# Kernel optimization log

Hardware: AMD Instinct MI355X
Metric: run time of the kernel (lower is better)

Reference implementation:

```python
import jax, jax.numpy as jnp
import numpy as np

END_CLAUSE, PRED, ARG_FUNC, ARG_VAR = 0, 1, 2, 3
NUM_ACTION_TYPES = 8
NUM_LAYERS = 3


def _ln(x, g, b, eps=1e-5):
    m = jnp.mean(x, -1, keepdims=True)
    v = jnp.var(x, -1, keepdims=True)
    return (x - m) * jax.lax.rsqrt(v + eps) * g + b


def _ssm_block(x, Win, b_in, Wdt, b_dt, Alog, WB, b_B, WC, b_C, Dp, Wout, b_out, g, b):
    # x: [B,T,D]
    res = x
    xz = x @ Win.T + b_in
    x_ssm, z = jnp.split(xz, 2, axis=-1)
    z = jax.nn.silu(z)
    dt = jax.nn.softplus(x_ssm @ Wdt.T + b_dt)   # [B,T,D]
    Bm = x_ssm @ WB.T + b_B                       # [B,T,N]
    Cm = x_ssm @ WC.T + b_C                       # [B,T,N]
    A = -jnp.exp(Alog)                            # [D,N]

    def step(h, inp):
        x_t, dt_t, B_t, C_t = inp                 # [B,D],[B,D],[B,N],[B,N]
        dA = jnp.exp(A[None] * dt_t[:, :, None])  # [B,D,N]
        h = dA * h + (dt_t * x_t)[:, :, None] * B_t[:, None, :]
        return h, jnp.einsum('bdn,bn->bd', h, C_t)

    h0 = jnp.zeros((x.shape[0], Alog.shape[0], Alog.shape[1]), x.dtype)
    xs = tuple(jnp.swapaxes(a, 0, 1) for a in (x_ssm, dt, Bm, Cm))
    _, ys = jax.lax.scan(step, h0, xs)
    y = jnp.swapaxes(ys, 0, 1)                    # [B,T,D]
    y = (y + Dp * x_ssm) * z
    y = y @ Wout.T + b_out
    return _ln(y + res, g, b)


def _forward(symbol_embeds, memory, action_embed, W_arg, b_arg, var_embed, W_comb, b_comb,
             Win, b_in, Wdt, b_dt, Alog, WB, b_B, WC, b_C, Dp, Wout, b_out, ssm_g, ssm_b,
             Wm, b_m, Wg, b_g, cn_g, cn_b, Wa, b_a, Wq, b_q, Wk, b_k, Wv, b_v,
             target_actions, target_arguments, symbol_mask):
    B, T = target_actions.shape
    S = symbol_embeds.shape[1]
    D = symbol_embeds.shape[2]
    MV = var_embed.shape[0]
    # teacher-forcing shift with END_CLAUSE BOS
    dec_a = jnp.concatenate([jnp.full((B, 1), END_CLAUSE, target_actions.dtype), target_actions[:, :-1]], 1)
    dec_g = jnp.concatenate([jnp.zeros((B, 1), target_arguments.dtype), target_arguments[:, :-1]], 1)
    act_emb = action_embed[dec_a]                                          # [B,T,D]
    sym = symbol_embeds[jnp.arange(B)[:, None], jnp.clip(dec_g, 0, S - 1)]  # [B,T,D]
    ptr_emb = sym @ W_arg.T + b_arg
    var_emb_t = var_embed[jnp.clip(dec_g, 0, MV - 1)]
    ptr_mask = (dec_a == PRED) | (dec_a == ARG_FUNC)
    vmask = dec_a == ARG_VAR
    arg_emb = jnp.where(ptr_mask[..., None], ptr_emb,
                        jnp.where(vmask[..., None], var_emb_t, jnp.zeros((), symbol_embeds.dtype)))
    h = jnp.concatenate([act_emb, arg_emb], -1) @ W_comb.T + b_comb
    mem_summary = memory.mean(1)  # zero padding included, matching torch code
    for l in range(NUM_LAYERS):
        h = _ssm_block(h, Win[l], b_in[l], Wdt[l], b_dt[l], Alog[l], WB[l], b_B[l], WC[l], b_C[l],
                       Dp[l], Wout[l], b_out[l], ssm_g[l], ssm_b[l])
        ctx = jnp.broadcast_to((mem_summary @ Wm[l].T + b_m[l])[:, None, :], h.shape)
        gate = jax.nn.sigmoid(jnp.concatenate([h, ctx], -1) @ Wg[l].T + b_g[l])
        h = _ln(h + gate * ctx, cn_g[l], cn_b[l])
    action_logits = h @ Wa.T + b_a
    scores = jnp.einsum('btd,bsd->bts', h @ Wq.T + b_q, symbol_embeds @ Wk.T + b_k) / (float(D) ** 0.5)
    scores = jnp.where(symbol_mask[:, None, :], scores, -jnp.inf)
    var_logits = h @ Wv.T + b_v
    return action_logits, scores, var_logits


def setup_inputs() -> dict:
    B, T, S, M, D, N, L, NA, MV = 8, 1024, 128, 512, 512, 16, NUM_LAYERS, NUM_ACTION_TYPES, 20
    keys = iter(jax.random.split(jax.random.key(0), 48))

    def nrm(shape, scale=1.0):
        return jax.random.normal(next(keys), shape, jnp.float32) * scale

    s = 1.0 / np.sqrt(D)
    s2 = 1.0 / np.sqrt(2 * D)
    inp = dict(
        symbol_embeds=nrm((B, S, D)), memory=nrm((B, M, D)),
        action_embed=nrm((NA, D), 0.02), W_arg=nrm((D, D), s), b_arg=jnp.zeros((D,)),
        var_embed=nrm((MV, D), 0.02), W_comb=nrm((D, 2 * D), s2), b_comb=jnp.zeros((D,)),
        Win=nrm((L, 2 * D, D), s), b_in=jnp.zeros((L, 2 * D)),
        Wdt=nrm((L, D, D), s), b_dt=jnp.zeros((L, D)),
        Alog=nrm((L, D, N)),
        WB=nrm((L, N, D), s), b_B=jnp.zeros((L, N)),
        WC=nrm((L, N, D), s), b_C=jnp.zeros((L, N)),
        Dp=jnp.ones((L, D)),
        Wout=nrm((L, D, D), s), b_out=jnp.zeros((L, D)),
        ssm_g=jnp.ones((L, D)), ssm_b=jnp.zeros((L, D)),
        Wm=nrm((L, D, D), s), b_m=jnp.zeros((L, D)),
        Wg=nrm((L, D, 2 * D), s2), b_g=jnp.zeros((L, D)),
        cn_g=jnp.ones((L, D)), cn_b=jnp.zeros((L, D)),
        Wa=nrm((NA, D), s), b_a=jnp.zeros((NA,)),
        Wq=nrm((D, D), s), b_q=jnp.zeros((D,)),
        Wk=nrm((D, D), s), b_k=jnp.zeros((D,)),
        Wv=nrm((MV, D), s), b_v=jnp.zeros((MV,)),
        target_actions=jax.random.randint(next(keys), (B, T), 0, NA),
        target_arguments=jax.random.randint(next(keys), (B, T), 0, S),
    )
    counts = jax.random.randint(next(keys), (B,), S // 2, S + 1)
    inp['symbol_mask'] = jnp.arange(S)[None, :] < counts[:, None]
    return inp


def reference(symbol_embeds, memory, action_embed, W_arg, b_arg, var_embed, W_comb, b_comb,
              Win, b_in, Wdt, b_dt, Alog, WB, b_B, WC, b_C, Dp, Wout, b_out, ssm_g, ssm_b,
              Wm, b_m, Wg, b_g, cn_g, cn_b, Wa, b_a, Wq, b_q, Wk, b_k, Wv, b_v,
              target_actions, target_arguments, symbol_mask):
    return _forward(symbol_embeds, memory, action_embed, W_arg, b_arg, var_embed, W_comb, b_comb,
                    Win, b_in, Wdt, b_dt, Alog, WB, b_B, WC, b_C, Dp, Wout, b_out, ssm_g, ssm_b,
                    Wm, b_m, Wg, b_g, cn_g, cn_b, Wa, b_a, Wq, b_q, Wk, b_k, Wv, b_v,
                    target_actions, target_arguments, symbol_mask)
```

## Files before the change

### kernel.cpp

```cpp
#include <hip/hip_runtime.h>
#include <math.h>

#define R_  8192
#define T_  1024
#define B_  8
#define S_  128
#define D_  512
#define N_  16
#define MV_ 20
#define NA_ 8
#define MM_ 512

#define TC  4
#define LCH 256
#define TS  32
#define DB  8
#define TP  36

typedef __attribute__((ext_vector_type(8))) short short8;
typedef __attribute__((ext_vector_type(4))) float f32x4;

static __device__ __forceinline__ float sigmoidf_(float x) {
  return 1.f / (1.f + __expf(-x));
}

static __device__ __forceinline__ void split2(float x0, float x1,
                                              unsigned& hp, unsigned& lp) {
  unsigned u0 = __float_as_uint(x0), u1 = __float_as_uint(x1);
  unsigned r0 = u0 + 0x7fffu + ((u0 >> 16) & 1u);
  unsigned r1 = u1 + 0x7fffu + ((u1 >> 16) & 1u);
  hp = __builtin_amdgcn_perm(r1, r0, 0x07060302u);
  float l0 = x0 - __uint_as_float(r0 & 0xffff0000u);
  float l1 = x1 - __uint_as_float(r1 & 0xffff0000u);
  lp = __builtin_amdgcn_perm(__float_as_uint(l1), __float_as_uint(l0),
                             0x07060302u);
}

#define KP 40

__global__ void __launch_bounds__(256) gemm_bx3(
    const float* __restrict__ A, int lda,
    const unsigned short* __restrict__ Wh, const unsigned short* __restrict__ Wl,
    const float* __restrict__ bias,
    const float* __restrict__ bbias,
    float* __restrict__ C, int ldc,
    int K, int act,
    float* __restrict__ aux1, float* __restrict__ aux2)
{
  __shared__ unsigned short Ah[128 * KP], Al[128 * KP];
  __shared__ unsigned short Bh[64 * KP],  Bl[64 * KP];
  const int tid = threadIdx.x;
  const int m0 = blockIdx.y << 7;
  const int n0 = blockIdx.x << 6;
  const int lane = tid & 63;
  const int wm = ((tid >> 6) & 1) << 6;
  const int wn = (tid >> 7) << 5;
  const int lr = lane & 15, quad = lane >> 4;

  const int arow = tid >> 1, akoff = (tid & 1) << 4;
  const float* ap = A + (size_t)(m0 + arow) * lda + akoff;
  const int brow = tid >> 2, bkoff = (tid & 3) << 3;
  const unsigned short* wph = Wh + (size_t)(n0 + brow) * K + bkoff;
  const unsigned short* wpl = Wl + (size_t)(n0 + brow) * K + bkoff;

  f32x4 acc[4][2];
#pragma unroll
  for (int mt = 0; mt < 4; ++mt)
#pragma unroll
    for (int nt = 0; nt < 2; ++nt)
      acc[mt][nt] = (f32x4){0.f, 0.f, 0.f, 0.f};

  for (int k0 = 0; k0 < K; k0 += 32) {
    float4 av[4];
#pragma unroll
    for (int i = 0; i < 4; ++i) av[i] = *(const float4*)(ap + k0 + (i << 2));
    uint4 bh = *(const uint4*)(wph + k0);
    uint4 bl = *(const uint4*)(wpl + k0);
    __syncthreads();
    {
      float af[16] = {av[0].x, av[0].y, av[0].z, av[0].w,
                      av[1].x, av[1].y, av[1].z, av[1].w,
                      av[2].x, av[2].y, av[2].z, av[2].w,
                      av[3].x, av[3].y, av[3].z, av[3].w};
#pragma unroll
      for (int g = 0; g < 2; ++g) {
        unsigned h4[4], l4[4];
#pragma unroll
        for (int p = 0; p < 4; ++p)
          split2(af[g * 8 + 2 * p], af[g * 8 + 2 * p + 1], h4[p], l4[p]);
        *(uint4*)&Ah[arow * KP + akoff + (g << 3)] = make_uint4(h4[0], h4[1], h4[2], h4[3]);
        *(uint4*)&Al[arow * KP + akoff + (g << 3)] = make_uint4(l4[0], l4[1], l4[2], l4[3]);
      }
    }
    *(uint4*)&Bh[brow * KP + bkoff] = bh;
    *(uint4*)&Bl[brow * KP + bkoff] = bl;
    __syncthreads();

    short8 fah[4], fal[4], fbh[2], fbl[2];
#pragma unroll
    for (int mt = 0; mt < 4; ++mt) {
      int r = (wm + mt * 16 + lr) * KP + quad * 8;
      fah[mt] = *(const short8*)&Ah[r];
      fal[mt] = *(const short8*)&Al[r];
    }
#pragma unroll
    for (int nt = 0; nt < 2; ++nt) {
      int r = (wn + nt * 16 + lr) * KP + quad * 8;
      fbh[nt] = *(const short8*)&Bh[r];
      fbl[nt] = *(const short8*)&Bl[r];
    }
#pragma unroll
    for (int mt = 0; mt < 4; ++mt)
#pragma unroll
      for (int nt = 0; nt < 2; ++nt) {
        acc[mt][nt] = __builtin_amdgcn_mfma_f32_16x16x32_bf16(
            fah[mt], fbl[nt], acc[mt][nt], 0, 0, 0);
        acc[mt][nt] = __builtin_amdgcn_mfma_f32_16x16x32_bf16(
            fal[mt], fbh[nt], acc[mt][nt], 0, 0, 0);
        acc[mt][nt] = __builtin_amdgcn_mfma_f32_16x16x32_bf16(
            fah[mt], fbh[nt], acc[mt][nt], 0, 0, 0);
      }
  }

  const int bb = m0 >> 10;
#pragma unroll
  for (int mt = 0; mt < 4; ++mt)
#pragma unroll
    for (int nt = 0; nt < 2; ++nt) {
      int ncol = n0 + wn + nt * 16 + lr;
      float bv = bias ? bias[ncol] : 0.f;
      if (bbias) bv += bbias[(size_t)bb * ldc + ncol];
#pragma unroll
      for (int reg = 0; reg < 4; ++reg) {
        int m = m0 + wm + mt * 16 + quad * 4 + reg;
        float v = acc[mt][nt][reg] + bv;
        if (act == 0) {
          C[(size_t)m * ldc + ncol] = v;
        } else if (act == 1) {
          C[(size_t)m * ldc + ncol] = (v > 20.f) ? v : log1pf(__expf(v));
        } else if (act == 2) {
          C[(size_t)m * ldc + ncol] = sigmoidf_(v);
        } else if (act == 3) {
          if (ncol < 512)      C[(size_t)m * 512 + ncol] = (v > 20.f) ? v : log1pf(__expf(v));
          else if (ncol < 528) aux1[(size_t)m * 16 + (ncol - 512)] = v;
          else if (ncol < 544) aux2[(size_t)m * 16 + (ncol - 528)] = v;
        } else {
          if (ncol < 512)      C[(size_t)m * 512 + ncol] = v;
          else if (ncol < 520) aux1[(size_t)m * 8 + (ncol - 512)] = v;
          else if (ncol < 540) aux2[(size_t)m * 20 + (ncol - 520)] = v;
        }
      }
    }
}

static __device__ __forceinline__ void wcvt_body(
    int gid, const float* __restrict__ W, int ldw,
    unsigned short* __restrict__ hi, unsigned short* __restrict__ lo)
{
  int base = gid << 3;
  int r = base >> 9, c = base & 511;
  const float* p = W + (size_t)r * ldw + c;
  float4 a0 = *(const float4*)p, a1 = *(const float4*)(p + 4);
  float af[8] = {a0.x, a0.y, a0.z, a0.w, a1.x, a1.y, a1.z, a1.w};
  unsigned h4[4], l4[4];
#pragma unroll
  for (int p2 = 0; p2 < 4; ++p2) split2(af[2 * p2], af[2 * p2 + 1], h4[p2], l4[p2]);
  *(uint4*)&hi[(size_t)r * 512 + c] = make_uint4(h4[0], h4[1], h4[2], h4[3]);
  *(uint4*)&lo[(size_t)r * 512 + c] = make_uint4(l4[0], l4[1], l4[2], l4[3]);
}

static __device__ __forceinline__ void pack_body(
    int gid, unsigned short* __restrict__ hi, unsigned short* __restrict__ lo,
    float* __restrict__ bd,
    const float* __restrict__ w0, const float* __restrict__ b0,
    const float* __restrict__ w1, const float* __restrict__ b1,
    const float* __restrict__ w2, const float* __restrict__ b2,
    int n1, int n2)
{
  int base = gid << 3;
  int r = base >> 9, c = base & 511;
  const float* src = nullptr;
  if (r < 512)                 src = w0 + (size_t)r * 512 + c;
// ... 38 lines not shown
                           const float* __restrict__ Wg_l,
                           unsigned short* WsqH, unsigned short* WsqL,
                           unsigned short* WgH, unsigned short* WgL)
{
  int blk = blockIdx.x;
  if (blk < 128)
    wcvt_body(blk * 256 + threadIdx.x, Wout_l, 512, WsqH, WsqL);
  else
    wcvt_body((blk - 128) * 256 + threadIdx.x, Wg_l, 1024, WgH, WgL);
}

__global__ void cvt_heads(const float* __restrict__ Wq, const float* __restrict__ b_q,
                          const float* __restrict__ Wa, const float* __restrict__ b_a,
                          const float* __restrict__ Wv, const float* __restrict__ b_v,
                          const float* __restrict__ Wk,
                          unsigned short* WpkH, unsigned short* WpkL, float* bpk,
                          unsigned short* WsqH, unsigned short* WsqL)
{
  int blk = blockIdx.x;
  if (blk < 144)
    pack_body(blk * 256 + threadIdx.x, WpkH, WpkL, bpk,
              Wq, b_q, Wa, b_a, Wv, b_v, NA_, MV_);
  else
    wcvt_body((blk - 144) * 256 + threadIdx.x, Wk, 512, WsqH, WsqL);
}

__global__ void wcvt(const float* __restrict__ W, int ldw,
                     unsigned short* __restrict__ hi, unsigned short* __restrict__ lo)
{
  wcvt_body(blockIdx.x * 256 + threadIdx.x, W, ldw, hi, lo);
}

#define BM 64
#define BN 64
#define BK 16

__global__ void __launch_bounds__(256) scores_kernel(
    const float* __restrict__ q, const float* __restrict__ kmat,
    const int* __restrict__ mask, float* __restrict__ out)
{
  __shared__ __align__(16) float As[BK][BM + 4];
  __shared__ __align__(16) float Ws[BK][BN + 4];
  const int b = blockIdx.z;
  const float* A = q + (size_t)b * T_ * D_;
  const float* W = kmat + (size_t)b * S_ * D_;
  const int tid = threadIdx.x;
  const int m0 = blockIdx.y * BM;
  const int n0 = blockIdx.x * BN;
  const int tx = tid & 15, ty = tid >> 4;
  const int lr = tid >> 2;
  const int lk = (tid & 3) << 2;
  float acc[4][4] = {{0.f}};
  const float* aptr = A + (size_t)(m0 + lr) * D_ + lk;
  const float* wptr = W + (size_t)(n0 + lr) * D_ + lk;

  for (int k0 = 0; k0 < D_; k0 += BK) {
    float4 av = *(const float4*)(aptr + k0);
    float4 wv = *(const float4*)(wptr + k0);
    __syncthreads();
    As[lk + 0][lr] = av.x; As[lk + 1][lr] = av.y;
    As[lk + 2][lr] = av.z; As[lk + 3][lr] = av.w;
    Ws[lk + 0][lr] = wv.x; Ws[lk + 1][lr] = wv.y;
    Ws[lk + 2][lr] = wv.z; Ws[lk + 3][lr] = wv.w;
    __syncthreads();
#pragma unroll
    for (int kk = 0; kk < BK; ++kk) {
      float4 a4 = *(const float4*)&As[kk][ty << 2];
      float4 b4 = *(const float4*)&Ws[kk][tx << 2];
      float a_[4] = {a4.x, a4.y, a4.z, a4.w};
      float b_[4] = {b4.x, b4.y, b4.z, b4.w};
#pragma unroll
      for (int i = 0; i < 4; ++i)
#pragma unroll
        for (int j = 0; j < 4; ++j)
          acc[i][j] = fmaf(a_[i], b_[j], acc[i][j]);
    }
  }

  const float scale = 0.044194173824159216f;
#pragma unroll
  for (int i = 0; i < 4; ++i) {
    int t = m0 + (ty << 2) + i;
#pragma unroll
    for (int j = 0; j < 4; ++j) {
      int s = n0 + (tx << 2) + j;
      float v = acc[i][j] * scale;
      if (mask[b * S_ + s] == 0) v = -1e30f;
      out[((size_t)(b * T_ + t)) * S_ + s] = v;
    }
  }
}

__global__ void gemm_small(const float* __restrict__ A, int lda,
                           const float* __restrict__ W, int ldw,
                           const float* __restrict__ bias,
                           float* __restrict__ C, int ldc,
                           int MN, int Ncols, int K)
{
  int gid = blockIdx.x * 256 + threadIdx.x;
// ... 35 lines not shown
  float acc = b_g[l * 512 + dd];
  for (int k = 0; k < 128; ++k) {
    float4 av = a[k], wv = w[k];
    acc = fmaf(av.x, wv.x, fmaf(av.y, wv.y, fmaf(av.z, wv.z, fmaf(av.w, wv.w, acc))));
  }
  gctx[gid] = acc;
}

__global__ void __launch_bounds__(256) transpose512(
    const float* __restrict__ A, float* __restrict__ At)
{
  __shared__ float tl[32][33];
  int i0 = blockIdx.y * 32, j0 = blockIdx.x * 32;
  int li = threadIdx.x & 31, lj = threadIdx.x >> 5;
#pragma unroll
  for (int k = 0; k < 4; ++k)
    tl[lj * 4 + k][li] = A[(size_t)(i0 + lj * 4 + k) * 512 + j0 + li];
  __syncthreads();
#pragma unroll
  for (int k = 0; k < 4; ++k)
    At[(size_t)(j0 + lj * 4 + k) * 512 + i0 + li] = tl[li][lj * 4 + k];
}

__global__ void memsum_kernel(const float* __restrict__ mem, float* __restrict__ out)
{
  int b = blockIdx.x >> 1;
  int d = ((blockIdx.x & 1) << 8) + threadIdx.x;
  const float* p = mem + (size_t)b * MM_ * D_ + d;
  float s = 0.f;
  for (int m = 0; m < MM_; ++m) s += p[(size_t)m * D_];
  out[b * D_ + d] = s * (1.f / MM_);
}

__global__ void combine_kernel(float* __restrict__ h, const float* __restrict__ Psym,
                               const float* __restrict__ Pact,
                               const float* __restrict__ Pvar, const float* __restrict__ b2,
                               const float* __restrict__ bcomb,
                               const int* __restrict__ ta, const int* __restrict__ tg)
{
  int i = blockIdx.x * 256 + threadIdx.x;
  int r = i >> 9, j = i & 511;
  int t = r & (T_ - 1);
  int a = t ? ta[r - 1] : 0;
  float val = Pact[a * D_ + j] + bcomb[j];
  if (a == 1 || a == 2) {
    int g = t ? tg[r - 1] : 0;
    g = g < 0 ? 0 : (g > S_ - 1 ? S_ - 1 : g);
    val += Psym[((size_t)(r >> 10) * S_ + g) * D_ + j] + b2[j];
  } else if (a == 3) {
    int g = t ? tg[r - 1] : 0;
    g = g < 0 ? 0 : (g > MV_ - 1 ? MV_ - 1 : g);
    val += Pvar[g * D_ + j];
  }
  h[i] = val;
}

__global__ void __launch_bounds__(128) scan_pass1(
    const float* __restrict__ xz, const float* __restrict__ dts,
    const float* __restrict__ Bmv, const float* __restrict__ Alog,
    float* __restrict__ aprod, float* __restrict__ hend)
{
  __shared__ __align__(16) float sdtT[DB][TP];
  __shared__ __align__(16) float sxT[DB][TP];
  __shared__ __align__(16) float sB[TS][16];
  const int tid = threadIdx.x;
  const int n = tid & 15, dl = tid >> 4;
  const int c = blockIdx.x, db = blockIdx.y, b = blockIdx.z;
  const int d = (db << 3) + dl;
  const int t0 = c * LCH;
  const int lrow = tid >> 2, lc2 = (tid & 3) << 1, bc4 = (tid & 3) << 2;

  float An = -__expf(Alog[d * N_ + n]);
  float hst = 0.f, dsum = 0.f;

  for (int tt = 0; tt < LCH; tt += TS) {
    __syncthreads();
    {
      size_t gr = (size_t)b * T_ + t0 + tt + lrow;
      float2 dt2 = *(const float2*)&dts[(gr << 9) + (db << 3) + lc2];
      float2 x2  = *(const float2*)&xz[(gr << 10) + (db << 3) + lc2];
      sdtT[lc2][lrow] = dt2.x; sdtT[lc2 + 1][lrow] = dt2.y;
      sxT[lc2][lrow]  = x2.x;  sxT[lc2 + 1][lrow]  = x2.y;
      *(float4*)&sB[lrow][bc4] = *(const float4*)&Bmv[gr * N_ + bc4];
    }
    __syncthreads();
    float dtr[TS], xr[TS];
#pragma unroll
    for (int qv = 0; qv < TS / 4; ++qv) {
      *(float4*)&dtr[qv << 2] = *(const float4*)&sdtT[dl][qv << 2];
      *(float4*)&xr[qv << 2]  = *(const float4*)&sxT[dl][qv << 2];
    }
#pragma unroll
    for (int s = 0; s < TS; ++s) {
      float Bv = sB[s][n];
      float dA = __expf(An * dtr[s]);
      hst = fmaf(dA, hst, dtr[s] * xr[s] * Bv);
      dsum += dtr[s];
    }
  }
  size_t idx = (size_t)c * (B_ * D_ * N_) + ((size_t)b * D_ + d) * N_ + n;
  aprod[idx] = __expf(An * dsum);
  hend[idx]  = hst;
}

__global__ void scan_pass2(const float* __restrict__ aprod, float* __restrict__ hs)
{
  int g = blockIdx.x * 256 + threadIdx.x;
  float prev = 0.f;
  for (int c = 0; c < TC; ++c) {
    size_t idx = (size_t)c * (B_ * D_ * N_) + g;
    float a = aprod[idx], he = hs[idx];
    hs[idx] = prev;
    prev = fmaf(a, prev, he);
  }
}

#define HPAD 20

__global__ void __launch_bounds__(128) scan_pass3(
    const float* __restrict__ xz, float* __restrict__ dy,
    const float* __restrict__ Bmv, const float* __restrict__ Cmv,
    const float* __restrict__ Alog, const float* __restrict__ hstart,
    const float* __restrict__ Dp)
{
  __shared__ __align__(16) float sdtT[DB][TP];
  __shared__ __align__(16) float sxT[DB][TP];
  __shared__ __align__(16) float szT[DB][TP];
  __shared__ __align__(16) float sB[TS][16];
  __shared__ __align__(16) float sC[TS][16];
  __shared__ __align__(16) float sterm[128][HPAD];
  const int tid = threadIdx.x;
  const int n = tid & 15, dl = tid >> 4;
  const int c = blockIdx.x, db = blockIdx.y, b = blockIdx.z;
  const int d = (db << 3) + dl;
  const int t0 = c * LCH;
  const int lrow = tid >> 2, lc2 = (tid & 3) << 1, bc4 = (tid & 3) << 2;
  const int rsi = tid >> 3, rdl = tid & 7;

  float An = -__expf(Alog[d * N_ + n]);
  float Dpr = Dp[(db << 3) + rdl];
  size_t sidx = (size_t)c * (B_ * D_ * N_) + ((size_t)b * D_ + d) * N_ + n;
  float hst = hstart[sidx];

  for (int tt = 0; tt < LCH; tt += TS) {
    __syncthreads();
    {
      size_t gr = (size_t)b * T_ + t0 + tt + lrow;
      float2 dt2 = *(const float2*)&dy[(gr << 9) + (db << 3) + lc2];
      float2 x2  = *(const float2*)&xz[(gr << 10) + (db << 3) + lc2];
      float2 z2  = *(const float2*)&xz[(gr << 10) + D_ + (db << 3) + lc2];
      sdtT[lc2][lrow] = dt2.x; sdtT[lc2 + 1][lrow] = dt2.y;
      sxT[lc2][lrow]  = x2.x;  sxT[lc2 + 1][lrow]  = x2.y;
      szT[lc2][lrow]  = z2.x;  szT[lc2 + 1][lrow]  = z2.y;
      *(float4*)&sB[lrow][bc4] = *(const float4*)&Bmv[gr * N_ + bc4];
      *(float4*)&sC[lrow][bc4] = *(const float4*)&Cmv[gr * N_ + bc4];
    }
    __syncthreads();
    float dtr[TS], xr[TS];
#pragma unroll
    for (int qv = 0; qv < TS / 4; ++qv) {
      *(float4*)&dtr[qv << 2] = *(const float4*)&sdtT[dl][qv << 2];
      *(float4*)&xr[qv << 2]  = *(const float4*)&sxT[dl][qv << 2];
    }
#pragma unroll
    for (int half = 0; half < 2; ++half) {
      const int hs = half << 4;
#pragma unroll
      for (int si = 0; si < 16; ++si) {
        int s = hs + si;
        float Bv = sB[s][n], Cv = sC[s][n];
        float dA = __expf(An * dtr[s]);
        hst = fmaf(dA, hst, dtr[s] * xr[s] * Bv);
        sterm[(si << 3) + dl][n] = hst * Cv;
      }
      __syncthreads();
      {
        float4 t0v = *(const float4*)&sterm[tid][0];
        float4 t1v = *(const float4*)&sterm[tid][4];
        float4 t2v = *(const float4*)&sterm[tid][8];
        float4 t3v = *(const float4*)&sterm[tid][12];
        float s16 = ((t0v.x + t0v.y) + (t0v.z + t0v.w))
                  + ((t1v.x + t1v.y) + (t1v.z + t1v.w))
                  + ((t2v.x + t2v.y) + (t2v.z + t2v.w))
                  + ((t3v.x + t3v.y) + (t3v.z + t3v.w));
        float zv = szT[rdl][hs + rsi];
        float xv = sxT[rdl][hs + rsi];
        float yv = (s16 + Dpr * xv) * (zv * sigmoidf_(zv));
        __syncthreads();
        sdtT[rdl][hs + rsi] = yv;
      }
      __syncthreads();
    }
    {
      size_t gr = (size_t)b * T_ + t0 + tt + lrow;
      float2 y2;
      y2.x = sdtT[lc2][lrow];
      y2.y = sdtT[lc2 + 1][lrow];
      *(float2*)&dy[(gr << 9) + (db << 3) + lc2] = y2;
    }
  }
}

__global__ void __launch_bounds__(256) ln_kernel(
    float* __restrict__ h, const float* __restrict__ add,
    const float* __restrict__ ctx,
    const float* __restrict__ gw, const float* __restrict__ bw, int mode)
{
  int r = (blockIdx.x << 2) + (threadIdx.x >> 6);
  int lane = threadIdx.x & 63;
  int b = r >> 10;
  size_t base = (size_t)r * D_;
  float v[8];
#pragma unroll
  for (int k = 0; k < 8; ++k) {
    int j = lane + (k << 6);
    float x = h[base + j];
    float a = add[base + j];
    v[k] = mode ? fmaf(a, ctx[b * D_ + j], x) : (x + a);
  }
  float s = 0.f;
#pragma unroll
  for (int k = 0; k < 8; ++k) s += v[k];
#pragma unroll
  for (int o = 1; o < 64; o <<= 1) s += __shfl_xor(s, o, 64);
  float mean = s * (1.f / D_);
  float vs = 0.f;
#pragma unroll
  for (int k = 0; k < 8; ++k) { float dv = v[k] - mean; vs = fmaf(dv, dv, vs); }
#pragma unroll
  for (int o = 1; o < 64; o <<= 1) vs += __shfl_xor(vs, o, 64);
  float inv = 1.0f / sqrtf(vs * (1.f / D_) + 1e-5f);
#pragma unroll
  for (int k = 0; k < 8; ++k) {
    int j = lane + (k << 6);
    h[base + j] = (v[k] - mean) * inv * gw[j] + bw[j];
  }
}

extern "C" void kernel_launch(void* const* d_in, const int* in_sizes, int n_in,
                              void* d_out, int out_size, void* d_ws, size_t ws_size,
                              hipStream_t stream)
{
  const float* symbol_embeds = (const float*)d_in[0];
  const float* memory_       = (const float*)d_in[1];
  const float* action_embed  = (const float*)d_in[2];
  const float* W_arg  = (const float*)d_in[3];
  const float* b_arg  = (const float*)d_in[4];
  const float* var_embed = (const float*)d_in[5];
  const float* W_comb = (const float*)d_in[6];
  const float* b_comb = (const float*)d_in[7];
  const float* Win  = (const float*)d_in[8];
  const float* b_in = (const float*)d_in[9];
  const float* Wdt  = (const float*)d_in[10];
  const float* b_dt = (const float*)d_in[11];
  const float* Alog = (const float*)d_in[12];
  const float* WB   = (const float*)d_in[13];
  const float* b_B  = (const float*)d_in[14];
  const float* WC   = (const float*)d_in[15];
  const float* b_C  = (const float*)d_in[16];
  const float* Dp   = (const float*)d_in[17];
  const float* Wout = (const float*)d_in[18];
  const float* b_out= (const float*)d_in[19];
  const float* ssm_g= (const float*)d_in[20];
  const float* ssm_b= (const float*)d_in[21];
  const float* Wm   = (const float*)d_in[22];
  const float* b_m  = (const float*)d_in[23];
  const float* Wg   = (const float*)d_in[24];
  const float* b_g  = (const float*)d_in[25];
  const float* cn_g = (const float*)d_in[26];
  const float* cn_b = (const float*)d_in[27];
  const float* Wa   = (const float*)d_in[28];
  const float* b_a  = (const float*)d_in[29];
  const float* Wq   = (const float*)d_in[30];
  const float* b_q  = (const float*)d_in[31];
  const float* Wk   = (const float*)d_in[32];
  const float* b_k  = (const float*)d_in[33];
  const float* Wv   = (const float*)d_in[34];
  const float* b_v  = (const float*)d_in[35];
  const int* ta     = (const int*)d_in[36];
  const int* tg     = (const int*)d_in[37];
  const int* smask  = (const int*)d_in[38];
  (void)in_sizes; (void)n_in; (void)out_size; (void)ws_size;

  float* ws = (float*)d_ws;
  float* xz = ws;
  float* dy = xz + (size_t)R_ * 1024;
  float* h  = dy + (size_t)R_ * 512;
  float* Psym = xz;

  float* out     = (float*)d_out;
  float* out_act = out;
  float* out_sc  = out + (size_t)R_ * NA_;
  float* out_var = out + (size_t)R_ * (NA_ + S_);

  float* Bmv  = out;
  float* Cmv  = Bmv  + 131072;
  float* aprd = Cmv  + 131072;
  float* hend = aprd + 262144;
  float* Wpk  = hend + 262144;
  float* bpk  = Wpk  + 294912;
  float* msum = bpk  + 576;
  float* ctxv = msum + 4096;
  float* gctx = ctxv + 12288;

  unsigned short* WpkH = (unsigned short*)Wpk;
  unsigned short* WpkL = WpkH + 294912;
  unsigned short* WinH = (unsigned short*)aprd;
  unsigned short* WinL = WinH + 524288;
  unsigned short* WsqH = (unsigned short*)aprd;
  unsigned short* WsqL = WsqH + 262144;
  unsigned short* WgH  = (unsigned short*)hend;
  unsigned short* WgL  = WgH + 262144;
  unsigned short* PrepH = (unsigned short*)Bmv;
  unsigned short* PrepL = PrepH + 262144;

  float* Pact = aprd;
  float* Pvar = Pact + 4096;
  float* b2   = Pvar + 10240;
  float* M2   = hend;
  float* WargT= Wpk;

  dim3 blk(256), blk128(128);

  memsum_kernel<<<16, blk, 0, stream>>>(memory_, msum);
  gemm_small<<<16, blk, 0, stream>>>(action_embed, 512, W_comb, 1024, nullptr,
                                     Pact, 512, 8 * 512, 512, 512);
  gemm_small<<<40, blk, 0, stream>>>(var_embed, 512, W_comb + 512, 1024, nullptr,
                                     Pvar, 512, 20 * 512, 512, 512);
  gemm_small<<<2, blk, 0, stream>>>(b_arg, 512, W_comb + 512, 1024, nullptr,
                                    b2, 512, 512, 512, 512);
  ctx_kernel<<<48, blk, 0, stream>>>(msum, Wm, b_m, ctxv);
  gctx_kernel<<<48, blk, 0, stream>>>(ctxv, Wg, b_g, gctx);
  transpose512<<<dim3(16, 16), blk, 0, stream>>>(W_arg, WargT);
  wcvt<<<128, blk, 0, stream>>>(WargT, 512, PrepH, PrepL);
  gemm_bx3<<<dim3(8, 4), blk, 0, stream>>>(W_comb + 512, 1024, PrepH, PrepL,
                                           nullptr, nullptr, M2, 512, 512, 0,
                                           nullptr, nullptr);
  wcvt<<<128, blk, 0, stream>>>(M2, 512, PrepH, PrepL);
  gemm_bx3<<<dim3(8, 8), blk, 0, stream>>>(symbol_embeds, 512, PrepH, PrepL,
                                           nullptr, nullptr, Psym, 512, 512, 0,
                                           nullptr, nullptr);
  combine_kernel<<<R_ * 512 / 256, blk, 0, stream>>>(h, Psym, Pact, Pvar, b2,
                                                     b_comb, ta, tg);

  for (int l = 0; l < 3; ++l) {
    const float* Win_l  = Win  + (size_t)l * 1024 * 512;
    const float* b_in_l = b_in + l * 1024;
    const float* Wdt_l  = Wdt  + (size_t)l * 512 * 512;
    const float* b_dt_l = b_dt + l * 512;
    const float* Alog_l = Alog + (size_t)l * 512 * 16;
    const float* WB_l   = WB   + (size_t)l * 16 * 512;
    const float* b_B_l  = b_B  + l * 16;
    const float* WC_l   = WC   + (size_t)l * 16 * 512;
    const float* b_C_l  = b_C  + l * 16;
    const float* Dp_l   = Dp   + l * 512;
    const float* Wout_l = Wout + (size_t)l * 512 * 512;
    const float* b_out_l= b_out+ l * 512;
    const float* ssm_g_l= ssm_g+ l * 512;
    const float* ssm_b_l= ssm_b+ l * 512;
    const float* Wg_l   = Wg   + (size_t)l * 512 * 1024;
    const float* cn_g_l = cn_g + l * 512;
    const float* cn_b_l = cn_b + l * 512;

    cvt_layerA<<<400, blk, 0, stream>>>(Win_l, Wdt_l, b_dt_l, WB_l, b_B_l,
                                        WC_l, b_C_l, WinH, WinL, WpkH, WpkL, bpk);
    gemm_bx3<<<dim3(16, 64), blk, 0, stream>>>(h, 512, WinH, WinL,
                                               b_in_l, nullptr, xz, 1024, 512, 0,
                                               nullptr, nullptr);
    gemm_bx3<<<dim3(9, 64), blk, 0, stream>>>(xz, 1024, WpkH, WpkL,
                                              bpk, nullptr, dy, 512, 512, 3,
                                              Bmv, Cmv);
    scan_pass1<<<dim3(TC, D_ / DB, B_), blk128, 0, stream>>>(xz, dy, Bmv, Alog_l,
                                                             aprd, hend);
    scan_pass2<<<B_ * D_ * N_ / 256, blk, 0, stream>>>(aprd, hend);
    scan_pass3<<<dim3(TC, D_ / DB, B_), blk128, 0, stream>>>(xz, dy, Bmv, Cmv,
                                                             Alog_l, hend, Dp_l);
    cvt_layerB<<<256, blk, 0, stream>>>(Wout_l, Wg_l, WsqH, WsqL, WgH, WgL);
    gemm_bx3<<<dim3(8, 64), blk, 0, stream>>>(dy, 512, WsqH, WsqL,
                                              b_out_l, nullptr, xz, 512, 512, 0,
                                              nullptr, nullptr);
    ln_kernel<<<2048, blk, 0, stream>>>(h, xz, nullptr, ssm_g_l, ssm_b_l, 0);
    gemm_bx3<<<dim3(8, 64), blk, 0, stream>>>(h, 512, WgH, WgL,
                                              nullptr, gctx + l * 4096, dy, 512, 512, 2,
                                              nullptr, nullptr);
    ln_kernel<<<2048, blk, 0, stream>>>(h, dy, ctxv + l * 4096, cn_g_l, cn_b_l, 1);
  }

  cvt_heads<<<272, blk, 0, stream>>>(Wq, b_q, Wa, b_a, Wv, b_v, Wk,
                                     WpkH, WpkL, bpk, WsqH, WsqL);
  gemm_bx3<<<dim3(9, 64), blk, 0, stream>>>(h, 512, WpkH, WpkL,
                                            bpk, nullptr, xz, 512, 512, 4,
                                            out_act, out_var);
  gemm_bx3<<<dim3(8, 8), blk, 0, stream>>>(symbol_embeds, 512, WsqH, WsqL,
                                           b_k, nullptr, dy, 512, 512, 0,
                                           nullptr, nullptr);
  scores_kernel<<<dim3(2, 16, 8), blk, 0, stream>>>(xz, dy, smask, out_sc);
}
```

Baseline: 1.171 ms.

## Store activations pre-split into bf16 hi/lo and widen GEMM tiles to 128

```diff
diff --git a/kernel.cpp b/kernel.cpp
--- a/kernel.cpp
+++ b/kernel.cpp
@@ -16,6 +16,7 @@
 #define TS  32
 #define DB  8
 #define TP  36
+#define KP  40
 
 typedef __attribute__((ext_vector_type(8))) short short8;
 typedef __attribute__((ext_vector_type(4))) float f32x4;
@@ -23,7 +24,13 @@
 static __device__ __forceinline__ float sigmoidf_(float x) {
   return 1.f / (1.f + __expf(-x));
 }
-
+static __device__ __forceinline__ void split1(float v, unsigned short& hi,
+                                              unsigned short& lo) {
+  unsigned u = __float_as_uint(v);
+  unsigned r = u + 0x7fffu + ((u >> 16) & 1u);
+  hi = (unsigned short)(r >> 16);
+  lo = (unsigned short)(__float_as_uint(v - __uint_as_float(r & 0xffff0000u)) >> 16);
+}
 static __device__ __forceinline__ void split2(float x0, float x1,
                                               unsigned& hp, unsigned& lp) {
   unsigned u0 = __float_as_uint(x0), u1 = __float_as_uint(x1);
@@ -35,68 +42,83 @@
   lp = __builtin_amdgcn_perm(__float_as_uint(l1), __float_as_uint(l0),
                              0x07060302u);
 }
-
-#define KP 40
-
-__global__ void __launch_bounds__(256) gemm_bx3(
-    const float* __restrict__ A, int lda,
+static __device__ __forceinline__ void recon2(unsigned hp, unsigned lp,
+                                              float& x0, float& x1) {
+  x0 = __uint_as_float(hp << 16) + __uint_as_float(lp << 16);
+  x1 = __uint_as_float(hp & 0xffff0000u) + __uint_as_float(lp & 0xffff0000u);
+}
+
+template<int BN>
+__global__ void __launch_bounds__(256) gemm_bb(
+    const unsigned short* __restrict__ Ahi, const unsigned short* __restrict__ Alo,
     const unsigned short* __restrict__ Wh, const unsigned short* __restrict__ Wl,
     const float* __restrict__ bias,
     const float* __restrict__ bbias,
     float* __restrict__ C, int ldc,
     int K, int act,
-    float* __restrict__ aux1, float* __restrict__ aux2)
+    float* __restrict__ aux1, float* __restrict__ aux2,
+    unsigned short* __restrict__ sp_hi, unsigned short* __restrict__ sp_lo)
 {
   __shared__ unsigned short Ah[128 * KP], Al[128 * KP];
-  __shared__ unsigned short Bh[64 * KP],  Bl[64 * KP];
+  __shared__ unsigned short Bh[BN * KP],  Bl[BN * KP];
   const int tid = threadIdx.x;
   const int m0 = blockIdx.y << 7;
-  const int n0 = blockIdx.x << 6;
+  const int n0 = blockIdx.x * BN;
   const int lane = tid & 63;
-  const int wm = ((tid >> 6) & 1) << 6;
-  const int wn = (tid >> 7) << 5;
+  const int widx = tid >> 6;
+  const int wm = (widx & 1) << 6;
+  const int wn = (widx >> 1) * (BN >> 1);
   const int lr = lane & 15, quad = lane >> 4;
+  const int NT = BN >> 5;
 
   const int arow = tid >> 1, akoff = (tid & 1) << 4;
-  const float* ap = A + (size_t)(m0 + arow) * lda + akoff;
-  const int brow = tid >> 2, bkoff = (tid & 3) << 3;
-  const unsigned short* wph = Wh + (size_t)(n0 + brow) * K + bkoff;
-  const unsigned short* wpl = Wl + (size_t)(n0 + brow) * K + bkoff;
-
-  f32x4 acc[4][2];
+  const unsigned short* aph = Ahi + (size_t)(m0 + arow) * K + akoff;
+  const unsigned short* apl = Alo + (size_t)(m0 + arow) * K + akoff;
+
+  f32x4 acc[4][4];
 #pragma unroll
   for (int mt = 0; mt < 4; ++mt)
 #pragma unroll
-    for (int nt = 0; nt < 2; ++nt)
+    for (int nt = 0; nt < NT; ++nt)
       acc[mt][nt] = (f32x4){0.f, 0.f, 0.f, 0.f};
 
   for (int k0 = 0; k0 < K; k0 += 32) {
-    float4 av[4];
-#pragma unroll
-    for (int i = 0; i < 4; ++i) av[i] = *(const float4*)(ap + k0 + (i << 2));
-    uint4 bh = *(const uint4*)(wph + k0);
-    uint4 bl = *(const uint4*)(wpl + k0);
+    uint4 ah0 = *(const uint4*)(aph + k0);
+    uint4 ah1 = *(const uint4*)(aph + k0 + 8);
+    uint4 al0 = *(const uint4*)(apl + k0);
+    uint4 al1 = *(const uint4*)(apl + k0 + 8);
+    uint4 bh0, bh1, bl0, bl1;
+    int brow, bkoff;
+    if (BN == 128) {
+      brow = tid >> 1; bkoff = (tid & 1) << 4;
+      const unsigned short* wph = Wh + (size_t)(n0 + brow) * K + bkoff;
+      const unsigned short* wpl = Wl + (size_t)(n0 + brow) * K + bkoff;
+      bh0 = *(const uint4*)(wph + k0); bh1 = *(const uint4*)(wph + k0 + 8);
+      bl0 = *(const uint4*)(wpl + k0); bl1 = *(const uint4*)(wpl + k0 + 8);
+    } else {
+      brow = tid >> 2; bkoff = (tid & 3) << 3;
+      const unsigned short* wph = Wh + (size_t)(n0 + brow) * K + bkoff;
+      const unsigned short* wpl = Wl + (size_t)(n0 + brow) * K + bkoff;
+      bh0 = *(const uint4*)(wph + k0);
+      bl0 = *(const uint4*)(wpl + k0);
+    }
     __syncthreads();
-    {
-      float af[16] = {av[0].x, av[0].y, av[0].z, av[0].w,
-                      av[1].x, av[1].y, av[1].z, av[1].w,
-                      av[2].x, av[2].y, av[2].z, av[2].w,
-                      av[3].x, av[3].y, av[3].z, av[3].w};
-#pragma unroll
-      for (int g = 0; g < 2; ++g) {
-        unsigned h4[4], l4[4];
-#pragma unroll
-        for (int p = 0; p < 4; ++p)
-          split2(af[g * 8 + 2 * p], af[g * 8 + 2 * p + 1], h4[p], l4[p]);
-        *(uint4*)&Ah[arow * KP + akoff + (g << 3)] = make_uint4(h4[0], h4[1], h4[2], h4[3]);
-        *(uint4*)&Al[arow * KP + akoff + (g << 3)] = make_uint4(l4[0], l4[1], l4[2], l4[3]);
-      }
-    }
-    *(uint4*)&Bh[brow * KP + bkoff] = bh;
-    *(uint4*)&Bl[brow * KP + bkoff] = bl;
+    *(uint4*)&Ah[arow * KP + akoff] = ah0;
+    *(uint4*)&Ah[arow * KP + akoff + 8] = ah1;
+    *(uint4*)&Al[arow * KP + akoff] = al0;
+    *(uint4*)&Al[arow * KP + akoff + 8] = al1;
+    if (BN == 128) {
+      *(uint4*)&Bh[brow * KP + bkoff] = bh0;
+      *(uint4*)&Bh[brow * KP + bkoff + 8] = bh1;
+      *(uint4*)&Bl[brow * KP + bkoff] = bl0;
+      *(uint4*)&Bl[brow * KP + bkoff + 8] = bl1;
+    } else {
+      *(uint4*)&Bh[brow * KP + bkoff] = bh0;
+      *(uint4*)&Bl[brow * KP + bkoff] = bl0;
+    }
     __syncthreads();
 
-    short8 fah[4], fal[4], fbh[2], fbl[2];
+    short8 fah[4], fal[4], fbh[4], fbl[4];
 #pragma unroll
     for (int mt = 0; mt < 4; ++mt) {
       int r = (wm + mt * 16 + lr) * KP + quad * 8;
@@ -104,7 +126,7 @@
       fal[mt] = *(const short8*)&Al[r];
     }
 #pragma unroll
-    for (int nt = 0; nt < 2; ++nt) {
+    for (int nt = 0; nt < NT; ++nt) {
       int r = (wn + nt * 16 + lr) * KP + quad * 8;
       fbh[nt] = *(const short8*)&Bh[r];
       fbl[nt] = *(const short8*)&Bl[r];
@@ -112,7 +134,7 @@
 #pragma unroll
     for (int mt = 0; mt < 4; ++mt)
 #pragma unroll
-      for (int nt = 0; nt < 2; ++nt) {
+      for (int nt = 0; nt < NT; ++nt) {
         acc[mt][nt] = __builtin_amdgcn_mfma_f32_16x16x32_bf16(
             fah[mt], fbl[nt], acc[mt][nt], 0, 0, 0);
         acc[mt][nt] = __builtin_amdgcn_mfma_f32_16x16x32_bf16(
@@ -126,7 +148,7 @@
 #pragma unroll
   for (int mt = 0; mt < 4; ++mt)
 #pragma unroll
-    for (int nt = 0; nt < 2; ++nt) {
+    for (int nt = 0; nt < NT; ++nt) {
       int ncol = n0 + wn + nt * 16 + lr;
       float bv = bias ? bias[ncol] : 0.f;
       if (bbias) bv += bbias[(size_t)bb * ldc + ncol];
@@ -136,18 +158,29 @@
         float v = acc[mt][nt][reg] + bv;
         if (act == 0) {
           C[(size_t)m * ldc + ncol] = v;
-        } else if (act == 1) {
-          C[(size_t)m * ldc + ncol] = (v > 20.f) ? v : log1pf(__expf(v));
         } else if (act == 2) {
           C[(size_t)m * ldc + ncol] = sigmoidf_(v);
         } else if (act == 3) {
-          if (ncol < 512)      C[(size_t)m * 512 + ncol] = (v > 20.f) ? v : log1pf(__expf(v));
+          if (ncol < 512) {
+            float sv = (v > 20.f) ? v : log1pf(__expf(v));
+            unsigned short hh, ll; split1(sv, hh, ll);
+            sp_hi[(size_t)m * 512 + ncol] = hh;
+            sp_lo[(size_t)m * 512 + ncol] = ll;
+          }
           else if (ncol < 528) aux1[(size_t)m * 16 + (ncol - 512)] = v;
           else if (ncol < 544) aux2[(size_t)m * 16 + (ncol - 528)] = v;
-        } else {
-          if (ncol < 512)      C[(size_t)m * 512 + ncol] = v;
+        } else if (act == 4) {
+          if (ncol < 512)      C[(size_t)m * ldc + ncol] = v;
           else if (ncol < 520) aux1[(size_t)m * 8 + (ncol - 512)] = v;
           else if (ncol < 540) aux2[(size_t)m * 20 + (ncol - 520)] = v;
+        } else {
+          if (ncol < 512) {
+            unsigned short hh, ll; split1(v, hh, ll);
+            sp_hi[(size_t)m * 512 + ncol] = hh;
+            sp_lo[(size_t)m * 512 + ncol] = ll;
+          } else {
+            aux2[(size_t)m * 512 + (ncol - 512)] = v;
+          }
         }
       }
     }
@@ -252,21 +285,21 @@
 }
 
 #define BM 64
-#define BN 64
-#define BK 16
+#define SBN 64
+#define SBK 16
 
 __global__ void __launch_bounds__(256) scores_kernel(
     const float* __restrict__ q, const float* __restrict__ kmat,
     const int* __restrict__ mask, float* __restrict__ out)
 {
-  __shared__ __align__(16) float As[BK][BM + 4];
-  __shared__ __align__(16) float Ws[BK][BN + 4];
+  __shared__ __align__(16) float As[SBK][BM + 4];
+  __shared__ __align__(16) float Ws[SBK][SBN + 4];
   const int b = blockIdx.z;
   const float* A = q + (size_t)b * T_ * D_;
   const float* W = kmat + (size_t)b * S_ * D_;
   const int tid = threadIdx.x;
   const int m0 = blockIdx.y * BM;
-  const int n0 = blockIdx.x * BN;
+  const int n0 = blockIdx.x * SBN;
   const int tx = tid & 15, ty = tid >> 4;
   const int lr = tid >> 2;
   const int lk = (tid & 3) << 2;
@@ -274,7 +307,7 @@
   const float* aptr = A + (size_t)(m0 + lr) * D_ + lk;
   const float* wptr = W + (size_t)(n0 + lr) * D_ + lk;
 
-  for (int k0 = 0; k0 < D_; k0 += BK) {
+  for (int k0 = 0; k0 < D_; k0 += SBK) {
     float4 av = *(const float4*)(aptr + k0);
     float4 wv = *(const float4*)(wptr + k0);
     __syncthreads();
@@ -284,7 +317,7 @@
     Ws[lk + 2][lr] = wv.z; Ws[lk + 3][lr] = wv.w;
     __syncthreads();
 #pragma unroll
-    for (int kk = 0; kk < BK; ++kk) {
+    for (int kk = 0; kk < SBK; ++kk) {
       float4 a4 = *(const float4*)&As[kk][ty << 2];
       float4 b4 = *(const float4*)&Ws[kk][tx << 2];
       float a_[4] = {a4.x, a4.y, a4.z, a4.w};
@@ -386,7 +419,10 @@
   out[b * D_ + d] = s * (1.f / MM_);
 }
 
-__global__ void combine_kernel(float* __restrict__ h, const float* __restrict__ Psym,
+__global__ void combine_kernel(float* __restrict__ h,
+                               unsigned short* __restrict__ sp_hi,
+                               unsigned short* __restrict__ sp_lo,
+                               const float* __restrict__ Psym,
                                const float* __restrict__ Pact,
                                const float* __restrict__ Pvar, const float* __restrict__ b2,
                                const float* __restrict__ bcomb,
@@ -407,10 +443,13 @@
     val += Pvar[g * D_ + j];
   }
   h[i] = val;
+  unsigned short hh, ll; split1(val, hh, ll);
+  sp_hi[i] = hh; sp_lo[i] = ll;
 }
 
 __global__ void __launch_bounds__(128) scan_pass1(
-    const float* __restrict__ xz, const float* __restrict__ dts,
+    const unsigned short* __restrict__ xhi, const unsigned short* __restrict__ xlo,
+    const unsigned short* __restrict__ dhi, const unsigned short* __restrict__ dlo,
     const float* __restrict__ Bmv, const float* __restrict__ Alog,
     float* __restrict__ aprod, float* __restrict__ hend)
 {
@@ -431,10 +470,16 @@
     __syncthreads();
     {
       size_t gr = (size_t)b * T_ + t0 + tt + lrow;
-      float2 dt2 = *(const float2*)&dts[(gr << 9) + (db << 3) + lc2];
-      float2 x2  = *(const float2*)&xz[(gr << 10) + (db << 3) + lc2];
-      sdtT[lc2][lrow] = dt2.x; sdtT[lc2 + 1][lrow] = dt2.y;
-      sxT[lc2][lrow]  = x2.x;  sxT[lc2 + 1][lrow]  = x2.y;
+      size_t ei = (gr << 9) + (db << 3) + lc2;
+      unsigned dh2 = *(const unsigned*)&dhi[ei];
+      unsigned dl2 = *(const unsigned*)&dlo[ei];
+      unsigned xh2 = *(const unsigned*)&xhi[ei];
+      unsigned xl2 = *(const unsigned*)&xlo[ei];
+      float d0, d1, x0, x1;
+      recon2(dh2, dl2, d0, d1);
+      recon2(xh2, xl2, x0, x1);
+      sdtT[lc2][lrow] = d0; sdtT[lc2 + 1][lrow] = d1;
+      sxT[lc2][lrow]  = x0; sxT[lc2 + 1][lrow]  = x1;
       *(float4*)&sB[lrow][bc4] = *(const float4*)&Bmv[gr * N_ + bc4];
     }
     __syncthreads();
@@ -472,7 +517,9 @@
 #define HPAD 20
 
 __global__ void __launch_bounds__(128) scan_pass3(
-    const float* __restrict__ xz, float* __restrict__ dy,
+    const unsigned short* __restrict__ xhi, const unsigned short* __restrict__ xlo,
+    unsigned short* __restrict__ dyhi, unsigned short* __restrict__ dylo,
+    const float* __restrict__ zreg,
     const float* __restrict__ Bmv, const float* __restrict__ Cmv,
     const float* __restrict__ Alog, const float* __restrict__ hstart,
     const float* __restrict__ Dp)
@@ -500,12 +547,18 @@
     __syncthreads();
     {
       size_t gr = (size_t)b * T_ + t0 + tt + lrow;
-      float2 dt2 = *(const float2*)&dy[(gr << 9) + (db << 3) + lc2];
-      float2 x2  = *(const float2*)&xz[(gr << 10) + (db << 3) + lc2];
-      float2 z2  = *(const float2*)&xz[(gr << 10) + D_ + (db << 3) + lc2];
-      sdtT[lc2][lrow] = dt2.x; sdtT[lc2 + 1][lrow] = dt2.y;
-      sxT[lc2][lrow]  = x2.x;  sxT[lc2 + 1][lrow]  = x2.y;
-      szT[lc2][lrow]  = z2.x;  szT[lc2 + 1][lrow]  = z2.y;
+      size_t ei = (gr << 9) + (db << 3) + lc2;
+      unsigned dh2 = *(const unsigned*)&dyhi[ei];
+      unsigned dl2 = *(const unsigned*)&dylo[ei];
+      unsigned xh2 = *(const unsigned*)&xhi[ei];
+      unsigned xl2 = *(const unsigned*)&xlo[ei];
+      float d0, d1, x0, x1;
+      recon2(dh2, dl2, d0, d1);
+      recon2(xh2, xl2, x0, x1);
+      float2 z2 = *(const float2*)&zreg[ei];
+      sdtT[lc2][lrow] = d0; sdtT[lc2 + 1][lrow] = d1;
+      sxT[lc2][lrow]  = x0; sxT[lc2 + 1][lrow]  = x1;
+      szT[lc2][lrow]  = z2.x; szT[lc2 + 1][lrow] = z2.y;
       *(float4*)&sB[lrow][bc4] = *(const float4*)&Bmv[gr * N_ + bc4];
       *(float4*)&sC[lrow][bc4] = *(const float4*)&Cmv[gr * N_ + bc4];
     }
@@ -547,16 +600,20 @@
     }
     {
       size_t gr = (size_t)b * T_ + t0 + tt + lrow;
-      float2 y2;
-      y2.x = sdtT[lc2][lrow];
-      y2.y = sdtT[lc2 + 1][lrow];
-      *(float2*)&dy[(gr << 9) + (db << 3) + lc2] = y2;
+      size_t ei = (gr << 9) + (db << 3) + lc2;
+      float y0 = sdtT[lc2][lrow], y1 = sdtT[lc2 + 1][lrow];
+      unsigned hp, lp;
+      split2(y0, y1, hp, lp);
+      *(unsigned*)&dyhi[ei] = hp;
+      *(unsigned*)&dylo[ei] = lp;
     }
   }
 }
 
 __global__ void __launch_bounds__(256) ln_kernel(
-    float* __restrict__ h, const float* __restrict__ add,
+    float* __restrict__ h,
+    unsigned short* __restrict__ sp_hi, unsigned short* __restrict__ sp_lo,
+    const float* __restrict__ add,
     const float* __restrict__ ctx,
     const float* __restrict__ gw, const float* __restrict__ bw, int mode)
 {
@@ -587,7 +644,10 @@
 #pragma unroll
   for (int k = 0; k < 8; ++k) {
     int j = lane + (k << 6);
-    h[base + j] = (v[k] - mean) * inv * gw[j] + bw[j];
+    float ov = (v[k] - mean) * inv * gw[j] + bw[j];
+    h[base + j] = ov;
+    unsigned short hh, ll; split1(ov, hh, ll);
+    sp_hi[base + j] = hh; sp_lo[base + j] = ll;
   }
 }
 
@@ -636,11 +696,16 @@
   const int* smask  = (const int*)d_in[38];
   (void)in_sizes; (void)n_in; (void)out_size; (void)ws_size;
 
+  const size_t RD = (size_t)R_ * 512;
+
   float* ws = (float*)d_ws;
-  float* xz = ws;
-  float* dy = xz + (size_t)R_ * 1024;
-  float* h  = dy + (size_t)R_ * 512;
-  float* Psym = xz;
+  unsigned short* xhi = (unsigned short*)ws;
+  unsigned short* xlo = xhi + RD;
+  float* regA = ws;
+  float* zreg = ws + RD;
+  unsigned short* csp_hi = (unsigned short*)(ws + 2 * RD);
+  unsigned short* csp_lo = csp_hi + RD;
+  float* h = ws + 3 * RD;
 
   float* out     = (float*)d_out;
   float* out_act = out;
@@ -660,7 +725,7 @@
   unsigned short* WpkH = (unsigned short*)Wpk;
   unsigned short* WpkL = WpkH + 294912;
   unsigned short* WinH = (unsigned short*)aprd;
-  unsigned short* WinL = WinH + 524288;
+  unsigned short* WinL = (unsigned short*)hend;
   unsigned short* WsqH = (unsigned short*)aprd;
   unsigned short* WsqL = WsqH + 262144;
   unsigned short* WgH  = (unsigned short*)hend;
@@ -687,15 +752,15 @@
   gctx_kernel<<<48, blk, 0, stream>>>(ctxv, Wg, b_g, gctx);
   transpose512<<<dim3(16, 16), blk, 0, stream>>>(W_arg, WargT);
   wcvt<<<128, blk, 0, stream>>>(WargT, 512, PrepH, PrepL);
-  gemm_bx3<<<dim3(8, 4), blk, 0, stream>>>(W_comb + 512, 1024, PrepH, PrepL,
-                                           nullptr, nullptr, M2, 512, 512, 0,
-                                           nullptr, nullptr);
+  wcvt<<<128, blk, 0, stream>>>(W_comb + 512, 1024, csp_hi, csp_lo);
+  gemm_bb<128><<<dim3(4, 4), blk, 0, stream>>>(csp_hi, csp_lo, PrepH, PrepL,
+      nullptr, nullptr, M2, 512, 512, 0, nullptr, nullptr, nullptr, nullptr);
   wcvt<<<128, blk, 0, stream>>>(M2, 512, PrepH, PrepL);
-  gemm_bx3<<<dim3(8, 8), blk, 0, stream>>>(symbol_embeds, 512, PrepH, PrepL,
-                                           nullptr, nullptr, Psym, 512, 512, 0,
-                                           nullptr, nullptr);
-  combine_kernel<<<R_ * 512 / 256, blk, 0, stream>>>(h, Psym, Pact, Pvar, b2,
-                                                     b_comb, ta, tg);
+  wcvt<<<256, blk, 0, stream>>>(symbol_embeds, 512, csp_hi, csp_lo);
+  gemm_bb<128><<<dim3(4, 8), blk, 0, stream>>>(csp_hi, csp_lo, PrepH, PrepL,
+      nullptr, nullptr, regA, 512, 512, 0, nullptr, nullptr, nullptr, nullptr);
+  combine_kernel<<<R_ * 512 / 256, blk, 0, stream>>>(h, csp_hi, csp_lo, regA,
+                                                     Pact, Pvar, b2, b_comb, ta, tg);
 
   for (int l = 0; l < 3; ++l) {
     const float* Win_l  = Win  + (size_t)l * 1024 * 512;
@@ -718,35 +783,32 @@
 
     cvt_layerA<<<400, blk, 0, stream>>>(Win_l, Wdt_l, b_dt_l, WB_l, b_B_l,
                                         WC_l, b_C_l, WinH, WinL, WpkH, WpkL, bpk);
-    gemm_bx3<<<dim3(16, 64), blk, 0, stream>>>(h, 512, WinH, WinL,
-                                               b_in_l, nullptr, xz, 1024, 512, 0,
-                                               nullptr, nullptr);
-    gemm_bx3<<<dim3(9, 64), blk, 0, stream>>>(xz, 1024, WpkH, WpkL,
-                                              bpk, nullptr, dy, 512, 512, 3,
-                                              Bmv, Cmv);
-    scan_pass1<<<dim3(TC, D_ / DB, B_), blk128, 0, stream>>>(xz, dy, Bmv, Alog_l,
-                                                             aprd, hend);
+    gemm_bb<128><<<dim3(8, 64), blk, 0, stream>>>(csp_hi, csp_lo, WinH, WinL,
+        b_in_l, nullptr, nullptr, 512, 512, 5, nullptr, zreg, xhi, xlo);
+    gemm_bb<64><<<dim3(9, 64), blk, 0, stream>>>(xhi, xlo, WpkH, WpkL,
+        bpk, nullptr, nullptr, 512, 512, 3, Bmv, Cmv, csp_hi, csp_lo);
+    scan_pass1<<<dim3(TC, D_ / DB, B_), blk128, 0, stream>>>(xhi, xlo,
+        csp_hi, csp_lo, Bmv, Alog_l, aprd, hend);
     scan_pass2<<<B_ * D_ * N_ / 256, blk, 0, stream>>>(aprd, hend);
-    scan_pass3<<<dim3(TC, D_ / DB, B_), blk128, 0, stream>>>(xz, dy, Bmv, Cmv,
-                                                             Alog_l, hend, Dp_l);
+    scan_pass3<<<dim3(TC, D_ / DB, B_), blk128, 0, stream>>>(xhi, xlo,
+        csp_hi, csp_lo, zreg, Bmv, Cmv, Alog_l, hend, Dp_l);
     cvt_layerB<<<256, blk, 0, stream>>>(Wout_l, Wg_l, WsqH, WsqL, WgH, WgL);
-    gemm_bx3<<<dim3(8, 64), blk, 0, stream>>>(dy, 512, WsqH, WsqL,
-                                              b_out_l, nullptr, xz, 512, 512, 0,
-                                              nullptr, nullptr);
-    ln_kernel<<<2048, blk, 0, stream>>>(h, xz, nullptr, ssm_g_l, ssm_b_l, 0);
-    gemm_bx3<<<dim3(8, 64), blk, 0, stream>>>(h, 512, WgH, WgL,
-                                              nullptr, gctx + l * 4096, dy, 512, 512, 2,
-                                              nullptr, nullptr);
-    ln_kernel<<<2048, blk, 0, stream>>>(h, dy, ctxv + l * 4096, cn_g_l, cn_b_l, 1);
+    gemm_bb<128><<<dim3(4, 64), blk, 0, stream>>>(csp_hi, csp_lo, WsqH, WsqL,
+        b_out_l, nullptr, regA, 512, 512, 0, nullptr, nullptr, nullptr, nullptr);
+    ln_kernel<<<2048, blk, 0, stream>>>(h, csp_hi, csp_lo, regA, nullptr,
+                                        ssm_g_l, ssm_b_l, 0);
+    gemm_bb<128><<<dim3(4, 64), blk, 0, stream>>>(csp_hi, csp_lo, WgH, WgL,
+        nullptr, gctx + l * 4096, regA, 512, 512, 2, nullptr, nullptr, nullptr, nullptr);
+    ln_kernel<<<2048, blk, 0, stream>>>(h, csp_hi, csp_lo, regA, ctxv + l * 4096,
+                                        cn_g_l, cn_b_l, 1);
   }
 
   cvt_heads<<<272, blk, 0, stream>>>(Wq, b_q, Wa, b_a, Wv, b_v, Wk,
                                      WpkH, WpkL, bpk, WsqH, WsqL);
-  gemm_bx3<<<dim3(9, 64), blk, 0, stream>>>(h, 512, WpkH, WpkL,
-                                            bpk, nullptr, xz, 512, 512, 4,
-                                            out_act, out_var);
-  gemm_bx3<<<dim3(8, 8), blk, 0, stream>>>(symbol_embeds, 512, WsqH, WsqL,
-                                           b_k, nullptr, dy, 512, 512, 0,
-                                           nullptr, nullptr);
-  scores_kernel<<<dim3(2, 16, 8), blk, 0, stream>>>(xz, dy, smask, out_sc);
-}
+  gemm_bb<64><<<dim3(9, 64), blk, 0, stream>>>(csp_hi, csp_lo, WpkH, WpkL,
+      bpk, nullptr, regA, 512, 512, 4, out_act, out_var, nullptr, nullptr);
+  wcvt<<<256, blk, 0, stream>>>(symbol_embeds, 512, csp_hi, csp_lo);
+  gemm_bb<128><<<dim3(4, 8), blk, 0, stream>>>(csp_hi, csp_lo, WsqH, WsqL,
+      b_k, nullptr, zreg, 512, 512, 0, nullptr, nullptr, nullptr, nullptr);
+  scores_kernel<<<dim3(2, 16, 8), blk, 0, stream>>>(regA, zreg, smask, out_sc);
+}
```

After: 1.369 ms. 17.0% more time.

## Prefetch next K-tile into registers and swizzle block order in split-bf16 GEMM

Applied to the files above, without the earlier changes.

```diff
diff --git a/kernel.cpp b/kernel.cpp
--- a/kernel.cpp
+++ b/kernel.cpp
@@ -16,6 +16,7 @@
 #define TS  32
 #define DB  8
 #define TP  36
+#define KP  40
 
 typedef __attribute__((ext_vector_type(8))) short short8;
 typedef __attribute__((ext_vector_type(4))) float f32x4;
@@ -36,8 +37,6 @@
                              0x07060302u);
 }
 
-#define KP 40
-
 __global__ void __launch_bounds__(256) gemm_bx3(
     const float* __restrict__ A, int lda,
     const unsigned short* __restrict__ Wh, const unsigned short* __restrict__ Wl,
@@ -50,8 +49,20 @@
   __shared__ unsigned short Ah[128 * KP], Al[128 * KP];
   __shared__ unsigned short Bh[64 * KP],  Bl[64 * KP];
   const int tid = threadIdx.x;
-  const int m0 = blockIdx.y << 7;
-  const int n0 = blockIdx.x << 6;
+
+  int bx = blockIdx.x, by = blockIdx.y;
+  {
+    int gx = gridDim.x, gy = gridDim.y;
+    if ((gy & 7) == 0) {
+      int id = by * gx + bx;
+      int slot = id >> 3, ypg = gy >> 3;
+      by = (id & 7) * ypg + (slot % ypg);
+      bx = slot / ypg;
+    }
+  }
+  const int m0 = by << 7;
+  const int n0 = bx << 6;
+
   const int lane = tid & 63;
   const int wm = ((tid >> 6) & 1) << 6;
   const int wn = (tid >> 7) << 5;
@@ -70,12 +81,14 @@
     for (int nt = 0; nt < 2; ++nt)
       acc[mt][nt] = (f32x4){0.f, 0.f, 0.f, 0.f};
 
+  float4 av[4];
+  uint4 bhC, blC;
+#pragma unroll
+  for (int i = 0; i < 4; ++i) av[i] = *(const float4*)(ap + (i << 2));
+  bhC = *(const uint4*)(wph);
+  blC = *(const uint4*)(wpl);
+
   for (int k0 = 0; k0 < K; k0 += 32) {
-    float4 av[4];
-#pragma unroll
-    for (int i = 0; i < 4; ++i) av[i] = *(const float4*)(ap + k0 + (i << 2));
-    uint4 bh = *(const uint4*)(wph + k0);
-    uint4 bl = *(const uint4*)(wpl + k0);
     __syncthreads();
     {
       float af[16] = {av[0].x, av[0].y, av[0].z, av[0].w,
@@ -92,9 +105,17 @@
         *(uint4*)&Al[arow * KP + akoff + (g << 3)] = make_uint4(l4[0], l4[1], l4[2], l4[3]);
       }
     }
-    *(uint4*)&Bh[brow * KP + bkoff] = bh;
-    *(uint4*)&Bl[brow * KP + bkoff] = bl;
+    *(uint4*)&Bh[brow * KP + bkoff] = bhC;
+    *(uint4*)&Bl[brow * KP + bkoff] = blC;
     __syncthreads();
+
+    if (k0 + 32 < K) {
+      int kn = k0 + 32;
+#pragma unroll
+      for (int i = 0; i < 4; ++i) av[i] = *(const float4*)(ap + kn + (i << 2));
+      bhC = *(const uint4*)(wph + kn);
+      blC = *(const uint4*)(wpl + kn);
+    }
 
     short8 fah[4], fal[4], fbh[2], fbl[2];
 #pragma unroll
```

After: 1.089 ms. 7.0% less time.
